# Performance work log

Hardware: AMD Instinct MI355X
Metric: run time of the kernel (lower is better)

Reference implementation:

```python
import jax, jax.numpy as jnp
import numpy as np
import math

N, C, L, D = 8, 16, 1024, 7   # x: [N, in_heads=C, L, in_features=D]
H = 16                        # out_heads
SZ = C * D                    # 112 (in_sz == out_sz since in_heads == out_heads)

def setup_inputs() -> dict:
    key = jax.random.key(0)
    ks = jax.random.split(key, 7)
    s = 1.0 / math.sqrt(SZ)
    return {
        "x":  jax.random.normal(ks[0], (N, C, L, D), dtype=jnp.float32),
        "Wq": jax.random.normal(ks[1], (SZ, SZ), dtype=jnp.float32) * s,
        "bq": jax.random.normal(ks[2], (SZ,), dtype=jnp.float32) * s,
        "Wk": jax.random.normal(ks[3], (SZ, SZ), dtype=jnp.float32) * s,
        "bk": jax.random.normal(ks[4], (SZ,), dtype=jnp.float32) * s,
        "Wv": jax.random.normal(ks[5], (SZ, SZ), dtype=jnp.float32) * s,
        "bv": jax.random.normal(ks[6], (SZ,), dtype=jnp.float32) * s,
    }

def _split_heads(t):
    # [N, L, H*d] -> [N, H, L, d]
    n, l, _ = t.shape
    return t.reshape(n, l, H, -1).transpose(0, 2, 1, 3)

def reference(x, Wq, bq, Wk, bk, Wv, bv):
    n, c, l, d = x.shape
    # [N, C, L, D] -> [N, L, C*D]
    xf = x.transpose(0, 2, 1, 3).reshape(n, l, c * d)
    q = _split_heads(xf @ Wq.T + bq)   # [N, H, L, d]
    k = _split_heads(xf @ Wk.T + bk)
    v = _split_heads(xf @ Wv.T + bv)
    scores = jnp.einsum('bhqd,bhkd->bhqk', q, k)
    # NOTE: original scales by sqrt(scores.shape[-1]) == sqrt(L), not sqrt(head_dim)
    scores = scores / jnp.sqrt(jnp.asarray(l, scores.dtype))
    weights = jax.nn.softmax(scores.astype(jnp.float32), axis=-1).astype(scores.dtype)
    # dropout p=0.5 is identity in eval mode
    return jnp.einsum('bhqk,bhkd->bhqd', weights, v)
```

## Files before the change

kernel.cpp:

```cpp
#include <hip/hip_runtime.h>
#include <math.h>

#define NB 8
#define CH 16
#define LL 1024
#define DD 7
#define HH 16

typedef float    v2f  __attribute__((ext_vector_type(2)));
typedef float    v4f  __attribute__((ext_vector_type(4)));
typedef float    v16f __attribute__((ext_vector_type(16)));
typedef short    v8s  __attribute__((ext_vector_type(8)));
typedef unsigned v4u  __attribute__((ext_vector_type(4)));

#if __has_builtin(__builtin_amdgcn_exp2f)
#define EXP2F(x) __builtin_amdgcn_exp2f(x)
#else
#define EXP2F(x) exp2f(x)
#endif

__device__ inline unsigned bf16_rne(float f) {
    unsigned u = __builtin_bit_cast(unsigned, f);
    return (u + 0x7fffu + ((u >> 16) & 1u)) >> 16;
}
__device__ inline unsigned pack_trunc(float a, float b) {
    unsigned ua = __builtin_bit_cast(unsigned, a);
    unsigned ub = __builtin_bit_cast(unsigned, b);
    return (ua >> 16) | (ub & 0xffff0000u);
}

__global__ __launch_bounds__(256, 2) void qkv_proj(
    const float* __restrict__ x,
    const float* __restrict__ Wq, const float* __restrict__ bq,
    const float* __restrict__ Wk, const float* __restrict__ bk,
    const float* __restrict__ Wv, const float* __restrict__ bv,
    unsigned short* __restrict__ qkvb)
{
    __shared__ __align__(16) unsigned short Wb[112 * 136];
    __shared__ __align__(16) unsigned short xb[64 * 136];

    int bx  = blockIdx.x;
    int mat = bx / (NB * 16);
    int rem = bx % (NB * 16);
    int n   = rem / 16;
    int l0  = (rem % 16) * 64;

    const float* W = (mat == 0) ? Wq : (mat == 1) ? Wk : Wv;
    const float* b = (mat == 0) ? bq : (mat == 1) ? bk : bv;

    int tid = threadIdx.x;

    {
        const float4* Wsrc = (const float4*)W;
        for (int i4 = tid; i4 < 3136; i4 += 256) {
            int j  = i4 / 28;
            int ii = (i4 - j * 28) * 4;
            float4 w = Wsrc[i4];
            unsigned lo = bf16_rne(w.x) | (bf16_rne(w.y) << 16);
            unsigned hi = bf16_rne(w.z) | (bf16_rne(w.w) << 16);
            *(uint2*)&Wb[j * 136 + ii] = make_uint2(lo, hi);
        }
    }
    for (int idx = tid; idx < 64 * 112; idx += 256) {
        int c  = idx / 448;
        int r  = idx - c * 448;
        int l  = r / 7;
        int dd = r - l * 7;
        xb[l * 136 + c * 7 + dd] =
            (unsigned short)bf16_rne(x[((n * CH + c) * LL + l0 + l) * DD + dd]);
    }
    for (int idx = tid; idx < 64 * 16; idx += 256)
        xb[(idx >> 4) * 136 + 112 + (idx & 15)] = 0;
    for (int idx = tid; idx < 112 * 16; idx += 256)
        Wb[(idx >> 4) * 136 + 112 + (idx & 15)] = 0;

    {
        size_t base = ((size_t)(mat * NB + n) * HH) * (LL * 8);
        for (int idx = tid; idx < 1024; idx += 256) {
            int hh = idx >> 6, l = idx & 63;
            qkvb[base + (size_t)(hh * LL + l0 + l) * 8 + 7] = 0;
        }
    }
    __syncthreads();

    int wv = tid >> 6, lane = tid & 63, l15 = lane & 15, l4 = lane >> 4;

    const unsigned short* Arow = xb + (wv * 16 + l15) * 136 + l4 * 8;
    v8s af[4];
    #pragma unroll
    for (int k4 = 0; k4 < 4; ++k4) af[k4] = *(const v8s*)(Arow + k4 * 32);

    v4f acc[7];
    #pragma unroll
    for (int jt = 0; jt < 7; ++jt) acc[jt] = (v4f){0.f, 0.f, 0.f, 0.f};

    #pragma unroll
    for (int jt = 0; jt < 7; ++jt) {
        const unsigned short* Brow = Wb + (jt * 16 + l15) * 136 + l4 * 8;
        #pragma unroll
        for (int k4 = 0; k4 < 4; ++k4) {
            v8s bf = *(const v8s*)(Brow + k4 * 32);
            acc[jt] = __builtin_amdgcn_mfma_f32_16x16x32_bf16(af[k4], bf, acc[jt], 0, 0, 0);
        }
    }

    const float scale = (mat == 0) ? 0.0450842200277801f  : 1.0f;
    size_t mbase = ((size_t)(mat * NB + n) * HH) * (LL * 8);
    #pragma unroll
    for (int jt = 0; jt < 7; ++jt) {
        int j   = jt * 16 + l15;
        int hh  = j / 7;
        int dim = j - hh * 7;
        float bj = b[j];
        int lrow = l0 + wv * 16 + l4 * 4;
        size_t rb = mbase + (size_t)hh * (LL * 8) + (size_t)lrow * 8 + dim;
        #pragma unroll
        for (int r = 0; r < 4; ++r) {
            float val = (acc[jt][r] + bj) * scale;
            qkvb[rb + (size_t)r * 8] = (unsigned short)bf16_rne(val);
        }
    }
}

__global__ __launch_bounds__(256, 2) void attn(
    const unsigned short* __restrict__ qkvb, float* __restrict__ out)
{
    __shared__ __align__(16) unsigned short Kl[LL * 8];
    __shared__ __align__(16) unsigned short Vt[8 * 1048];

    int bx = blockIdx.x;
    int qt = bx & 3, h = (bx >> 2) & 15, n = bx >> 6;
    int tid  = threadIdx.x;
    int wave = tid >> 6, lane = tid & 63;
    int l31 = lane & 31, g5 = lane >> 5;

    const unsigned short* Qg = qkvb + (size_t)((0 * NB + n) * HH + h) * (LL * 8);
    const unsigned short* Kg = qkvb + (size_t)((1 * NB + n) * HH + h) * (LL * 8);
    const unsigned short* Vg = qkvb + (size_t)((2 * NB + n) * HH + h) * (LL * 8);

    {
        const uint4* Ks = (const uint4*)Kg;
        uint4* Kd = (uint4*)Kl;
        #pragma unroll
        for (int it = 0; it < 4; ++it) Kd[tid + it * 256] = Ks[tid + it * 256];
    }
    {
        const uint4* Vs = (const uint4*)Vg;
        uint4 r0 = Vs[4 * tid], r1 = Vs[4 * tid + 1];
        uint4 r2 = Vs[4 * tid + 2], r3 = Vs[4 * tid + 3];
        const unsigned* p0 = (const unsigned*)&r0;
        const unsigned* p1 = (const unsigned*)&r1;
        const unsigned* p2 = (const unsigned*)&r2;
        const unsigned* p3 = (const unsigned*)&r3;
        int col = ((tid >> 3) << 5) + ((tid & 1) << 3) + (((tid >> 1) & 1) << 2)
                + (((tid >> 2) & 1) << 4);
        #pragma unroll
        for (int d = 0; d < 7; ++d) {
            unsigned a0 = p0[d >> 1], a1 = p1[d >> 1], a2 = p2[d >> 1], a3 = p3[d >> 1];
            unsigned w0, w1;
            if (d & 1) { w0 = (a0 >> 16) | (a1 & 0xffff0000u); w1 = (a2 >> 16) | (a3 & 0xffff0000u); }
            else       { w0 = (a0 & 0xffffu) | (a1 << 16);     w1 = (a2 & 0xffffu) | (a3 << 16); }
            *(uint2*)&Vt[d * 1048 + col] = make_uint2(w0, w1);
        }
        *(uint2*)&Vt[7 * 1048 + col] = make_uint2(0x3f803f80u, 0x3f803f80u);
    }
    __syncthreads();

    int q0 = qt * 256 + wave * 64 + l31;
    v8s zero8 = {0, 0, 0, 0, 0, 0, 0, 0};
    v8s qfA = (lane < 32) ? *(const v8s*)(Qg + (size_t)q0 * 8)        : zero8;
    v8s qfB = (lane < 32) ? *(const v8s*)(Qg + (size_t)(q0 + 32) * 8) : zero8;

    const unsigned short* Vrow = Vt + (l31 & 7) * 1048 + g5 * 8;
    v16f accA = {}, accB = {};

    v8s kf = (lane < 32) ? *(const v8s*)(Kl + l31 * 8) : zero8;

    #pragma unroll 2
    for (int c = 0; c < 32; ++c) {
        v16f sA = __builtin_amdgcn_mfma_f32_32x32x16_bf16(kf, qfA, (v16f){}, 0, 0, 0);
        v16f sB = __builtin_amdgcn_mfma_f32_32x32x16_bf16(kf, qfB, (v16f){}, 0, 0, 0);
        if (c < 31)
            kf = (lane < 32) ? *(const v8s*)(Kl + ((c + 1) * 32 + l31) * 8) : zero8;
        v8s va1 = *(const v8s*)(Vrow + c * 32);
        v8s va2 = *(const v8s*)(Vrow + c * 32 + 16);

        unsigned pkA[8], pkB[8];
        #pragma unroll
        for (int p = 0; p < 8; ++p)
            pkA[p] = pack_trunc(EXP2F(sA[2 * p]), EXP2F(sA[2 * p + 1]));
        #pragma unroll
        for (int p = 0; p < 8; ++p)
            pkB[p] = pack_trunc(EXP2F(sB[2 * p]), EXP2F(sB[2 * p + 1]));

        v8s pA1 = __builtin_bit_cast(v8s, (v4u){pkA[0], pkA[1], pkA[2], pkA[3]});
        v8s pA2 = __builtin_bit_cast(v8s, (v4u){pkA[4], pkA[5], pkA[6], pkA[7]});
        v8s pB1 = __builtin_bit_cast(v8s, (v4u){pkB[0], pkB[1], pkB[2], pkB[3]});
        v8s pB2 = __builtin_bit_cast(v8s, (v4u){pkB[4], pkB[5], pkB[6], pkB[7]});

        accA = __builtin_amdgcn_mfma_f32_32x32x16_bf16(va1, pA1, accA, 0, 0, 0);
        accA = __builtin_amdgcn_mfma_f32_32x32x16_bf16(va2, pA2, accA, 0, 0, 0);
        accB = __builtin_amdgcn_mfma_f32_32x32x16_bf16(va1, pB1, accB, 0, 0, 0);
        accB = __builtin_amdgcn_mfma_f32_32x32x16_bf16(va2, pB2, accB, 0, 0, 0);
    }

    size_t hb = (size_t)(n * HH + h) * LL * 7;
    {
        float rs = __shfl(accA[3], 32 + l31, 64);
        float* base = out + hb + (size_t)q0 * 7;
        #pragma unroll
        for (int r = 0; r < 4; ++r) {
            int dim = 4 * g5 + r;
            if (dim < 7) base[dim] = accA[r] / rs;
        }
    }
    {
        float rs = __shfl(accB[3], 32 + l31, 64);
        float* base = out + hb + (size_t)(q0 + 32) * 7;
        #pragma unroll
        for (int r = 0; r < 4; ++r) {
            int dim = 4 * g5 + r;
            if (dim < 7) base[dim] = accB[r] / rs;
        }
    }
}

extern "C" void kernel_launch(void* const* d_in, const int* in_sizes, int n_in,
                              void* d_out, int out_size, void* d_ws, size_t ws_size,
                              hipStream_t stream) {
    const float* x  = (const float*)d_in[0];
    const float* Wq = (const float*)d_in[1];
    const float* bq = (const float*)d_in[2];
    const float* Wk = (const float*)d_in[3];
    const float* bk = (const float*)d_in[4];
    const float* Wv = (const float*)d_in[5];
    const float* bv = (const float*)d_in[6];
    unsigned short* qkvb = (unsigned short*)d_ws;
    float* o = (float*)d_out;

    qkv_proj<<<dim3(3 * NB * 16), dim3(256), 0, stream>>>(x, Wq, bq, Wk, bk, Wv, bv, qkvb);
    attn<<<dim3(NB * HH * 4), dim3(256), 0, stream>>>(qkvb, o);
}
```

Measured before the change: 100.6 us.

## Split attention key range across two wave groups with LDS reduction

Doubles the attention block to 512 threads and splits the 1024 keys into two halves, each handled by four waves for the same query rows. The partial P·V accumulators from the second half are written to shared memory and summed by the first half before normalisation and the store. This is meant to raise the number of active waves per CU and halve the serial key loop per wave. In exchange it adds a reduction buffer, an extra barrier, and idle waves during the epilogue.

```diff
diff --git a/kernel.cpp b/kernel.cpp
--- a/kernel.cpp
+++ b/kernel.cpp
@@ -122,17 +122,20 @@
     }
 }
 
-__global__ __launch_bounds__(256, 2) void attn(
+__global__ __launch_bounds__(512, 4) void attn(
     const unsigned short* __restrict__ qkvb, float* __restrict__ out)
 {
     __shared__ __align__(16) unsigned short Kl[LL * 8];
     __shared__ __align__(16) unsigned short Vt[8 * 1048];
+    __shared__ __align__(16) float red[256 * 8];
 
     int bx = blockIdx.x;
     int qt = bx & 3, h = (bx >> 2) & 15, n = bx >> 6;
     int tid  = threadIdx.x;
     int wave = tid >> 6, lane = tid & 63;
     int l31 = lane & 31, g5 = lane >> 5;
+    int g  = wave & 3;
+    int kh = wave >> 2;
 
     const unsigned short* Qg = qkvb + (size_t)((0 * NB + n) * HH + h) * (LL * 8);
     const unsigned short* Kg = qkvb + (size_t)((1 * NB + n) * HH + h) * (LL * 8);
@@ -141,10 +144,10 @@
     {
         const uint4* Ks = (const uint4*)Kg;
         uint4* Kd = (uint4*)Kl;
-        #pragma unroll
-        for (int it = 0; it < 4; ++it) Kd[tid + it * 256] = Ks[tid + it * 256];
-    }
-    {
+        Kd[tid]       = Ks[tid];
+        Kd[tid + 512] = Ks[tid + 512];
+    }
+    if (tid < 256) {
         const uint4* Vs = (const uint4*)Vg;
         uint4 r0 = Vs[4 * tid], r1 = Vs[4 * tid + 1];
         uint4 r2 = Vs[4 * tid + 2], r3 = Vs[4 * tid + 3];
@@ -166,7 +169,7 @@
     }
     __syncthreads();
 
-    int q0 = qt * 256 + wave * 64 + l31;
+    int q0 = qt * 256 + g * 64 + l31;
     v8s zero8 = {0, 0, 0, 0, 0, 0, 0, 0};
     v8s qfA = (lane < 32) ? *(const v8s*)(Qg + (size_t)q0 * 8)        : zero8;
     v8s qfB = (lane < 32) ? *(const v8s*)(Qg + (size_t)(q0 + 32) * 8) : zero8;
@@ -174,16 +177,17 @@
     const unsigned short* Vrow = Vt + (l31 & 7) * 1048 + g5 * 8;
     v16f accA = {}, accB = {};
 
-    v8s kf = (lane < 32) ? *(const v8s*)(Kl + l31 * 8) : zero8;
+    int kbase = kh * 512;
+    v8s kf = (lane < 32) ? *(const v8s*)(Kl + (kbase + l31) * 8) : zero8;
 
     #pragma unroll 2
-    for (int c = 0; c < 32; ++c) {
+    for (int c = 0; c < 16; ++c) {
         v16f sA = __builtin_amdgcn_mfma_f32_32x32x16_bf16(kf, qfA, (v16f){}, 0, 0, 0);
         v16f sB = __builtin_amdgcn_mfma_f32_32x32x16_bf16(kf, qfB, (v16f){}, 0, 0, 0);
-        if (c < 31)
-            kf = (lane < 32) ? *(const v8s*)(Kl + ((c + 1) * 32 + l31) * 8) : zero8;
-        v8s va1 = *(const v8s*)(Vrow + c * 32);
-        v8s va2 = *(const v8s*)(Vrow + c * 32 + 16);
+        if (c < 15)
+            kf = (lane < 32) ? *(const v8s*)(Kl + (kbase + (c + 1) * 32 + l31) * 8) : zero8;
+        v8s va1 = *(const v8s*)(Vrow + (kbase + c * 32));
+        v8s va2 = *(const v8s*)(Vrow + (kbase + c * 32) + 16);
 
         unsigned pkA[8], pkB[8];
         #pragma unroll
@@ -204,23 +208,37 @@
         accB = __builtin_amdgcn_mfma_f32_32x32x16_bf16(va2, pB2, accB, 0, 0, 0);
     }
 
-    size_t hb = (size_t)(n * HH + h) * LL * 7;
-    {
-        float rs = __shfl(accA[3], 32 + l31, 64);
-        float* base = out + hb + (size_t)q0 * 7;
-        #pragma unroll
-        for (int r = 0; r < 4; ++r) {
-            int dim = 4 * g5 + r;
-            if (dim < 7) base[dim] = accA[r] / rs;
-        }
-    }
-    {
-        float rs = __shfl(accB[3], 32 + l31, 64);
-        float* base = out + hb + (size_t)(q0 + 32) * 7;
-        #pragma unroll
-        for (int r = 0; r < 4; ++r) {
-            int dim = 4 * g5 + r;
-            if (dim < 7) base[dim] = accB[r] / rs;
+    if (kh == 1) {
+        *(float4*)&red[(size_t)(g * 64 + l31) * 8 + 4 * g5] =
+            make_float4(accA[0], accA[1], accA[2], accA[3]);
+        *(float4*)&red[(size_t)(g * 64 + 32 + l31) * 8 + 4 * g5] =
+            make_float4(accB[0], accB[1], accB[2], accB[3]);
+    }
+    __syncthreads();
+    if (kh == 0) {
+        float4 pa = *(const float4*)&red[(size_t)(g * 64 + l31) * 8 + 4 * g5];
+        float4 pb = *(const float4*)&red[(size_t)(g * 64 + 32 + l31) * 8 + 4 * g5];
+        accA[0] += pa.x; accA[1] += pa.y; accA[2] += pa.z; accA[3] += pa.w;
+        accB[0] += pb.x; accB[1] += pb.y; accB[2] += pb.z; accB[3] += pb.w;
+
+        size_t hb = (size_t)(n * HH + h) * LL * 7;
+        {
+            float rs = __shfl(accA[3], 32 + l31, 64);
+            float* base = out + hb + (size_t)q0 * 7;
+            #pragma unroll
+            for (int r = 0; r < 4; ++r) {
+                int dim = 4 * g5 + r;
+                if (dim < 7) base[dim] = accA[r] / rs;
+            }
+        }
+        {
+            float rs = __shfl(accB[3], 32 + l31, 64);
+            float* base = out + hb + (size_t)(q0 + 32) * 7;
+            #pragma unroll
+            for (int r = 0; r < 4; ++r) {
+                int dim = 4 * g5 + r;
+                if (dim < 7) base[dim] = accB[r] / rs;
+            }
         }
     }
 }
@@ -239,5 +257,5 @@
     float* o = (float*)d_out;
 
     qkv_proj<<<dim3(3 * NB * 16), dim3(256), 0, stream>>>(x, Wq, bq, Wk, bk, Wv, bv, qkvb);
-    attn<<<dim3(NB * HH * 4), dim3(256), 0, stream>>>(qkvb, o);
-}
+    attn<<<dim3(NB * HH * 4), dim3(512), 0, stream>>>(qkvb, o);
+}
```

Result: no change. 99.47 us (-1.1%).
